# Kernel optimization log

Measured on AMD Instinct MI355X. Metric: run time of the kernel, lower is better.

The kernel has to match this reference:

```python
import jax, jax.numpy as jnp
import numpy as np

IN_FEATURES = 4096
OUT_FEATURES = 16384
BATCH, SEQ = 4, 2048


def setup_inputs() -> dict:
    key = jax.random.key(0)
    k_x, k_w, k_b = jax.random.split(key, 3)
    x = jax.random.normal(k_x, (BATCH, SEQ, IN_FEATURES), dtype=jnp.float32)
    # int8-valued quantized weight stored as int32 for portability (values in [-128, 127])
    weight_quantized = jax.random.randint(k_w, (OUT_FEATURES, IN_FEATURES), -128, 128, dtype=jnp.int32)
    weight_scale = jnp.float32(0.01)        # scalar scale (symmetric quant)
    weight_zero_point = jnp.float32(0.0)    # scalar zero point
    bias = jax.random.normal(k_b, (OUT_FEATURES,), dtype=jnp.float32)
    return {
        "x": x,
        "weight_quantized": weight_quantized,
        "weight_scale": weight_scale,
        "weight_zero_point": weight_zero_point,
        "bias": bias,
    }


def reference(x, weight_quantized, weight_scale, weight_zero_point, bias):
    # dequantize: (q - zero_point) * scale  -> fp32 weight [out, in]
    weight = (weight_quantized.astype(jnp.float32) - weight_zero_point) * weight_scale
    # F.linear: y = x @ W^T + b ; x: [b, s, in], W: [out, in] -> y: [b, s, out]
    return jnp.einsum("bsi,oi->bso", x, weight) + bias
```

## Files before the change

### kernel.cpp

```cpp
#include <hip/hip_runtime.h>
#include <hip/hip_bf16.h>
#include <cstdint>


#define M_DIM 8192
#define N_DIM 16384
#define K_DIM 4096
#define BK    128
#define NT    (K_DIM / BK)

using i32x4 = __attribute__((ext_vector_type(4))) int;

__global__ __launch_bounds__(256) void quant_x_kernel(const float* __restrict__ x,
                                                      signed char* __restrict__ xq,
                                                      float* __restrict__ rs1,
                                                      float* __restrict__ rs2) {
    const int row = blockIdx.x;
    const float* xr = x + (size_t)row * K_DIM;
    const int tid = threadIdx.x;

    float4 v[4];
    float amax = 0.f;
    #pragma unroll
    for (int j = 0; j < 4; ++j) {
        v[j] = *(const float4*)(xr + j * 1024 + tid * 4);
        amax = fmaxf(amax, fmaxf(fmaxf(fabsf(v[j].x), fabsf(v[j].y)),
                                 fmaxf(fabsf(v[j].z), fabsf(v[j].w))));
    }
    #pragma unroll
    for (int off = 32; off > 0; off >>= 1)
        amax = fmaxf(amax, __shfl_xor(amax, off));
    __shared__ float smax[4];
    __shared__ int   ssum[4];
    const int wv = tid >> 6, ln = tid & 63;
    if (ln == 0) smax[wv] = amax;
    __syncthreads();
    amax = fmaxf(fmaxf(smax[0], smax[1]), fmaxf(smax[2], smax[3]));
    const float s   = amax * (1.0f / 127.0f);
    const float inv = amax > 0.f ? 127.0f / amax : 0.f;

    int sum = 0;
    #pragma unroll
    for (int j = 0; j < 4; ++j) {
        int q0 = (int)__builtin_rintf(v[j].x * inv);
        int q1 = (int)__builtin_rintf(v[j].y * inv);
        int q2 = (int)__builtin_rintf(v[j].z * inv);
        int q3 = (int)__builtin_rintf(v[j].w * inv);
        sum += q0 + q1 + q2 + q3;
        int packed = (q0 & 255) | ((q1 & 255) << 8) | ((q2 & 255) << 16) | ((q3 & 255) << 24);
        *(int*)(xq + (size_t)row * K_DIM + j * 1024 + tid * 4) = packed;
    }
    #pragma unroll
    for (int off = 32; off > 0; off >>= 1)
        sum += __shfl_xor(sum, off);
    if (ln == 0) ssum[wv] = sum;
    __syncthreads();
    if (tid == 0) {
        int t = ssum[0] + ssum[1] + ssum[2] + ssum[3];
        rs1[row] = s;
        rs2[row] = s * (float)t;
    }
}

__global__ void quant_w_kernel(const int* __restrict__ q, signed char* __restrict__ o,
                               long long n) {
    long long i = ((long long)blockIdx.x * blockDim.x + threadIdx.x) * 4;
    const long long stride = (long long)gridDim.x * blockDim.x * 4;
    for (; i < n; i += stride) {
        int4 v = *(const int4*)(q + i);
        int packed = (v.x & 255) | ((v.y & 255) << 8) | ((v.z & 255) << 16) | ((v.w & 255) << 24);
        *(int*)(o + i) = packed;
    }
}

#define SB() __builtin_amdgcn_sched_barrier(0)

__device__ __forceinline__ void barrier_() {
    SB();
    asm volatile("" ::: "memory");
    __builtin_amdgcn_s_barrier();
    asm volatile("" ::: "memory");
    SB();
}

__device__ __forceinline__ void stage_half(const signed char* g0, unsigned char* l0) {
    __builtin_amdgcn_global_load_lds((const __attribute__((address_space(1))) void*)g0,
                                     (__attribute__((address_space(3))) void*)l0, 16, 0, 0);
    __builtin_amdgcn_global_load_lds(
        (const __attribute__((address_space(1))) void*)(g0 + (size_t)64 * K_DIM),
        (__attribute__((address_space(3))) void*)(l0 + 8192), 16, 0, 0);
}

__global__ __launch_bounds__(512, 2) void gemm_i8_kernel(const signed char* __restrict__ A,
                                                         const signed char* __restrict__ B,
                                                         const float* __restrict__ rs1,
                                                         const float* __restrict__ rs2,
                                                         const float* __restrict__ scale,
                                                         const float* __restrict__ zpp,
                                                         const float* __restrict__ bias,
                                                         float* __restrict__ C) {
    extern __shared__ unsigned char smem[];

    const int tid  = threadIdx.x;
    const int wave = tid >> 6;
    const int lane = tid & 63;
    const int fr = lane & 15, kq = lane >> 4;
    const int wr = wave >> 2, wc = wave & 3;

    const int swz = (blockIdx.x & 7) * 256 + (blockIdx.x >> 3);
    const int ntn = N_DIM / 256;
    const int tileRow = (swz / ntn) * 256;
    const int tileCol = (swz % ntn) * 256;

    const size_t goff = (size_t)(tid >> 3) * K_DIM + (((tid & 7) ^ ((tid >> 3) & 7)) * 16);
    const signed char* Au  = A + (size_t)tileRow * K_DIM + goff;
    const signed char* Bu  = B + (size_t)tileCol * K_DIM + goff;
    const signed char* AuH = Au + (size_t)128 * K_DIM;
    const signed char* BuH = Bu + (size_t)128 * K_DIM;

    const int aoffB = wr * 16384 + fr * 128;
    const int boffB = 32768 + wc * 8192 + fr * 128;
    int cs[2];
    #pragma unroll
    for (int ks = 0; ks < 2; ++ks)
        cs[ks] = ((ks * 4 + kq) ^ (fr & 7)) * 16;

    i32x4 acc[8][4] = {};
    i32x4 arA[4][2], arB[4][2], b0r[2][2], b1r[2][2];

    {
        unsigned char* w0 = smem + wave * 1024;
        unsigned char* w1 = smem + 65536 + wave * 1024;
        stage_half(Au,  w0);
        stage_half(AuH, w0 + 16384);
        stage_half(Bu,  w0 + 32768);
        stage_half(BuH, w0 + 49152);
        stage_half(Bu + BK,  w1 + 32768);
        stage_half(BuH + BK, w1 + 49152);
        stage_half(Au + BK,  w1);
    }
    SB();
    asm volatile("s_waitcnt vmcnt(6)" ::: "memory");
    barrier_();
    #pragma unroll
    for (int m = 0; m < 4; ++m)
        #pragma unroll
        for (int ks = 0; ks < 2; ++ks)
            arA[m][ks] = *(const i32x4*)(smem + aoffB + m * 2048 + cs[ks]);
    #pragma unroll
    for (int n = 0; n < 2; ++n)
        #pragma unroll
        for (int ks = 0; ks < 2; ++ks)
            b0r[n][ks] = *(const i32x4*)(smem + boffB + n * 2048 + cs[ks]);
    SB();

    for (int t = 0; t < NT; ++t) {
        const unsigned char* sbr = smem + (t & 1) * 65536;
        const unsigned char* nxr = smem + ((t + 1) & 1) * 65536;
        unsigned char* sbw = smem + (t & 1) * 65536 + wave * 1024;
        unsigned char* nxw = smem + ((t + 1) & 1) * 65536 + wave * 1024;
        const int kn1 = (t + 1) * BK, kn2 = (t + 2) * BK;

        if (t + 1 < NT) stage_half(AuH + kn1, nxw + 16384);
        #pragma unroll
        for (int n = 0; n < 2; ++n)
            #pragma unroll
            for (int ks = 0; ks < 2; ++ks)
                b1r[n][ks] = *(const i32x4*)(sbr + boffB + (n + 2) * 2048 + cs[ks]);
        SB();
        asm volatile("s_waitcnt lgkmcnt(4)" ::: "memory");
        SB();
        __builtin_amdgcn_s_setprio(1);
        #pragma unroll
        for (int ks = 0; ks < 2; ++ks)
            #pragma unroll
            for (int m = 0; m < 4; ++m)
                #pragma unroll
                for (int n = 0; n < 2; ++n)
                    acc[m][n] = __builtin_amdgcn_mfma_i32_16x16x64_i8(arA[m][ks], b0r[n][ks], acc[m][n], 0, 0, 0);
        __builtin_amdgcn_s_setprio(0);
        barrier_();

        #pragma unroll
        for (int m = 0; m < 4; ++m)
            #pragma unroll
            for (int ks = 0; ks < 2; ++ks)
                arB[m][ks] = *(const i32x4*)(sbr + aoffB + (m + 4) * 2048 + cs[ks]);
        SB();
        asm volatile("s_waitcnt lgkmcnt(8)" ::: "memory");
        SB();
        __builtin_amdgcn_s_setprio(1);
        #pragma unroll
        for (int ks = 0; ks < 2; ++ks)
            #pragma unroll
            for (int m = 0; m < 4; ++m)
                #pragma unroll
                for (int n = 0; n < 2; ++n)
                    acc[m][n + 2] = __builtin_amdgcn_mfma_i32_16x16x64_i8(arA[m][ks], b1r[n][ks], acc[m][n + 2], 0, 0, 0);
        __builtin_amdgcn_s_setprio(0);
        barrier_();

        if (t + 2 < NT) {
            stage_half(Bu + kn2,  sbw + 32768);
            stage_half(BuH + kn2, sbw + 49152);
        }
        SB();
        asm volatile("s_waitcnt lgkmcnt(0)" ::: "memory");
        SB();
        __builtin_amdgcn_s_setprio(1);
        #pragma unroll
        for (int ks = 0; ks < 2; ++ks)
            #pragma unroll
            for (int m = 0; m < 4; ++m)
                #pragma unroll
                for (int n = 0; n < 2; ++n)
                    acc[m + 4][n + 2] = __builtin_amdgcn_mfma_i32_16x16x64_i8(arB[m][ks], b1r[n][ks], acc[m + 4][n + 2], 0, 0, 0);
        __builtin_amdgcn_s_setprio(0);
        SB();
        if (t + 2 < NT) {
            asm volatile("s_waitcnt vmcnt(4)" ::: "memory");
        } else if (t + 1 < NT) {
            asm volatile("s_waitcnt vmcnt(0)" ::: "memory");
        }
        barrier_();

        if (t + 1 < NT) {
            #pragma unroll
            for (int m = 0; m < 4; ++m)
                #pragma unroll
                for (int ks = 0; ks < 2; ++ks)
                    arA[m][ks] = *(const i32x4*)(nxr + aoffB + m * 2048 + cs[ks]);
        }
        if (t + 2 < NT) stage_half(Au + kn2, sbw);
        SB();
        __builtin_amdgcn_s_setprio(1);
        #pragma unroll
        for (int ks = 0; ks < 2; ++ks)
            #pragma unroll
            for (int m = 0; m < 4; ++m)
                #pragma unroll
                for (int n = 0; n < 2; ++n)
                    acc[m + 4][n] = __builtin_amdgcn_mfma_i32_16x16x64_i8(arB[m][ks], b0r[n][ks], acc[m + 4][n], 0, 0, 0);
        __builtin_amdgcn_s_setprio(0);
        if (t + 1 < NT) {
            #pragma unroll
            for (int n = 0; n < 2; ++n)
                #pragma unroll
                for (int ks = 0; ks < 2; ++ks)
                    b0r[n][ks] = *(const i32x4*)(nxr + boffB + n * 2048 + cs[ks]);
        }
        SB();
        barrier_();
    }

    const float sw  = scale[0];
    const float zpv = zpp[0];
    float bv[4];
    #pragma unroll
    for (int n = 0; n < 4; ++n)
        bv[n] = bias[tileCol + wc * 64 + n * 16 + fr];
    #pragma unroll
    for (int m = 0; m < 8; ++m) {
        #pragma unroll
        for (int j = 0; j < 4; ++j) {
            const int grow = tileRow + wr * 128 + m * 16 + kq * 4 + j;
            const float f1 = rs1[grow] * sw;
            const float f2 = zpv * rs2[grow] * sw;
            float* Crow = C + (size_t)grow * N_DIM + tileCol + wc * 64 + fr;
            #pragma unroll
            for (int n = 0; n < 4; ++n)
                Crow[n * 16] = f1 * (float)acc[m][n][j] - f2 + bv[n];
        }
    }
}

__global__ void gemm_naive(const float* __restrict__ x, const int* __restrict__ wq,
                           const float* __restrict__ sp, const float* __restrict__ zp,
                           const float* __restrict__ bias, float* __restrict__ out) {
    __shared__ float sX[32][33];
    __shared__ float sW[32][33];
    const float s = sp[0], z = zp[0];
    const int tx = threadIdx.x & 15, ty = threadIdx.x >> 4;
    const int row0 = blockIdx.y * 32, col0 = blockIdx.x * 32;
    float acc[2][2] = {};
    for (int k0 = 0; k0 < K_DIM; k0 += 32) {
        for (int i = threadIdx.x; i < 32 * 32; i += 256) {
            int r = i >> 5, cc2 = i & 31;
            sX[r][cc2] = x[(size_t)(row0 + r) * K_DIM + k0 + cc2];
            sW[r][cc2] = ((float)wq[(size_t)(col0 + r) * K_DIM + k0 + cc2] - z) * s;
        }
        __syncthreads();
        #pragma unroll
        for (int k = 0; k < 32; ++k) {
            float xa0 = sX[ty * 2][k], xa1 = sX[ty * 2 + 1][k];
            float wb0 = sW[tx * 2][k], wb1 = sW[tx * 2 + 1][k];
            acc[0][0] += xa0 * wb0; acc[0][1] += xa0 * wb1;
            acc[1][0] += xa1 * wb0; acc[1][1] += xa1 * wb1;
        }
        __syncthreads();
    }
    #pragma unroll
    for (int i = 0; i < 2; ++i)
        #pragma unroll
        for (int j = 0; j < 2; ++j)
            out[(size_t)(row0 + ty * 2 + i) * N_DIM + (col0 + tx * 2 + j)] =
                acc[i][j] + bias[col0 + tx * 2 + j];
}

extern "C" void kernel_launch(void* const* d_in, const int* in_sizes, int n_in,
                              void* d_out, int out_size, void* d_ws, size_t ws_size,
                              hipStream_t stream) {
    const float* x     = (const float*)d_in[0];
    const int*   wq    = (const int*)d_in[1];
    const float* scale = (const float*)d_in[2];
    const float* zp    = (const float*)d_in[3];
    const float* bias  = (const float*)d_in[4];
    float* out = (float*)d_out;

    const size_t offXq = 0;
    const size_t offWq = (size_t)M_DIM * K_DIM;
    const size_t offR1 = offWq + (size_t)N_DIM * K_DIM;
    const size_t offR2 = offR1 + (size_t)M_DIM * sizeof(float);
    const size_t need  = offR2 + (size_t)M_DIM * sizeof(float);

    if (ws_size >= need) {
        signed char* xq  = (signed char*)d_ws + offXq;
        signed char* wq8 = (signed char*)d_ws + offWq;
        float* rs1 = (float*)((char*)d_ws + offR1);
        float* rs2 = (float*)((char*)d_ws + offR2);
        quant_x_kernel<<<M_DIM, 256, 0, stream>>>(x, xq, rs1, rs2);
        quant_w_kernel<<<4096, 256, 0, stream>>>(wq, wq8, (long long)N_DIM * K_DIM);
        (void)hipFuncSetAttribute((const void*)gemm_i8_kernel,
                                  hipFuncAttributeMaxDynamicSharedMemorySize, 131072);
        gemm_i8_kernel<<<(M_DIM / 256) * (N_DIM / 256), 512, 131072, stream>>>(
            xq, wq8, rs1, rs2, scale, zp, bias, out);
    } else {
        dim3 grid(N_DIM / 32, M_DIM / 32);
        gemm_naive<<<grid, 256, 0, stream>>>(x, wq, scale, zp, bias, out);
    }
}
```

Before: 640.3 us.

## Load B fragments directly from global into registers, bypassing LDS, and remap tile grid

The weight (B) operand is no longer staged through shared memory. Each wave loads its own MFMA B fragments straight from global memory into registers one k-tile ahead, which halves LDS use to 64 KB and removes the B LDS reads and writes. The tile mapping is also changed so each XCD owns a contiguous band of output columns, with rows varying fastest, to improve L2 reuse of B. In exchange, B global loads are no longer shared within the block: the four wave-rows read duplicate data, so B traffic into L1/L2 rises and the loads are small strided 16-byte reads. The vmcnt waits are reworked to match the new load counts.

```diff
diff --git a/kernel.cpp b/kernel.cpp
--- a/kernel.cpp
+++ b/kernel.cpp
@@ -107,68 +107,69 @@
     const int fr = lane & 15, kq = lane >> 4;
     const int wr = wave >> 2, wc = wave & 3;
 
-    const int swz = (blockIdx.x & 7) * 256 + (blockIdx.x >> 3);
-    const int ntn = N_DIM / 256;
-    const int tileRow = (swz / ntn) * 256;
-    const int tileCol = (swz % ntn) * 256;
+    const int xcd = blockIdx.x & 7, idx = blockIdx.x >> 3;
+    const int tileRow = (idx & 31) * 256;
+    const int tileCol = (xcd * 8 + (idx >> 5)) * 256;
 
     const size_t goff = (size_t)(tid >> 3) * K_DIM + (((tid & 7) ^ ((tid >> 3) & 7)) * 16);
     const signed char* Au  = A + (size_t)tileRow * K_DIM + goff;
-    const signed char* Bu  = B + (size_t)tileCol * K_DIM + goff;
     const signed char* AuH = Au + (size_t)128 * K_DIM;
-    const signed char* BuH = Bu + (size_t)128 * K_DIM;
 
     const int aoffB = wr * 16384 + fr * 128;
-    const int boffB = 32768 + wc * 8192 + fr * 128;
     int cs[2];
     #pragma unroll
     for (int ks = 0; ks < 2; ++ks)
         cs[ks] = ((ks * 4 + kq) ^ (fr & 7)) * 16;
 
+    const signed char* Bv = B + (size_t)(tileCol + wc * 64 + fr) * K_DIM + kq * 16;
+
     i32x4 acc[8][4] = {};
-    i32x4 arA[4][2], arB[4][2], b0r[2][2], b1r[2][2];
+    i32x4 arA[4][2], arB[4][2], bg0[2][2], bg1[2][2];
 
     {
         unsigned char* w0 = smem + wave * 1024;
-        unsigned char* w1 = smem + 65536 + wave * 1024;
+        unsigned char* w1 = smem + 32768 + wave * 1024;
         stage_half(Au,  w0);
         stage_half(AuH, w0 + 16384);
-        stage_half(Bu,  w0 + 32768);
-        stage_half(BuH, w0 + 49152);
-        stage_half(Bu + BK,  w1 + 32768);
-        stage_half(BuH + BK, w1 + 49152);
-        stage_half(Au + BK,  w1);
+        SB();
+        #pragma unroll
+        for (int n = 0; n < 2; ++n)
+            #pragma unroll
+            for (int ks = 0; ks < 2; ++ks)
+                bg0[n][ks] = *(const i32x4*)(Bv + (size_t)(n) * 16 * K_DIM + ks * 64);
+        #pragma unroll
+        for (int n = 0; n < 2; ++n)
+            #pragma unroll
+            for (int ks = 0; ks < 2; ++ks)
+                bg1[n][ks] = *(const i32x4*)(Bv + (size_t)(n + 2) * 16 * K_DIM + ks * 64);
+        SB();
+        stage_half(Au + BK, w1);
     }
     SB();
-    asm volatile("s_waitcnt vmcnt(6)" ::: "memory");
+    asm volatile("s_waitcnt vmcnt(10)" ::: "memory");
     barrier_();
     #pragma unroll
     for (int m = 0; m < 4; ++m)
         #pragma unroll
         for (int ks = 0; ks < 2; ++ks)
             arA[m][ks] = *(const i32x4*)(smem + aoffB + m * 2048 + cs[ks]);
-    #pragma unroll
-    for (int n = 0; n < 2; ++n)
-        #pragma unroll
-        for (int ks = 0; ks < 2; ++ks)
-            b0r[n][ks] = *(const i32x4*)(smem + boffB + n * 2048 + cs[ks]);
     SB();
 
     for (int t = 0; t < NT; ++t) {
-        const unsigned char* sbr = smem + (t & 1) * 65536;
-        const unsigned char* nxr = smem + ((t + 1) & 1) * 65536;
-        unsigned char* sbw = smem + (t & 1) * 65536 + wave * 1024;
-        unsigned char* nxw = smem + ((t + 1) & 1) * 65536 + wave * 1024;
+        const unsigned char* sbr = smem + (t & 1) * 32768;
+        const unsigned char* nxr = smem + ((t + 1) & 1) * 32768;
+        unsigned char* sbw = smem + (t & 1) * 32768 + wave * 1024;
+        unsigned char* nxw = smem + ((t + 1) & 1) * 32768 + wave * 1024;
         const int kn1 = (t + 1) * BK, kn2 = (t + 2) * BK;
 
         if (t + 1 < NT) stage_half(AuH + kn1, nxw + 16384);
-        #pragma unroll
-        for (int n = 0; n < 2; ++n)
-            #pragma unroll
-            for (int ks = 0; ks < 2; ++ks)
-                b1r[n][ks] = *(const i32x4*)(sbr + boffB + (n + 2) * 2048 + cs[ks]);
-        SB();
-        asm volatile("s_waitcnt lgkmcnt(4)" ::: "memory");
+        SB();
+        asm volatile("s_waitcnt lgkmcnt(0)" ::: "memory");
+        if (t + 1 < NT) {
+            asm volatile("s_waitcnt vmcnt(8)" ::: "memory");
+        } else {
+            asm volatile("s_waitcnt vmcnt(4)" ::: "memory");
+        }
         SB();
         __builtin_amdgcn_s_setprio(1);
         #pragma unroll
@@ -177,7 +178,7 @@
             for (int m = 0; m < 4; ++m)
                 #pragma unroll
                 for (int n = 0; n < 2; ++n)
-                    acc[m][n] = __builtin_amdgcn_mfma_i32_16x16x64_i8(arA[m][ks], b0r[n][ks], acc[m][n], 0, 0, 0);
+                    acc[m][n] = __builtin_amdgcn_mfma_i32_16x16x64_i8(arA[m][ks], bg0[n][ks], acc[m][n], 0, 0, 0);
         __builtin_amdgcn_s_setprio(0);
         barrier_();
 
@@ -187,7 +188,11 @@
             for (int ks = 0; ks < 2; ++ks)
                 arB[m][ks] = *(const i32x4*)(sbr + aoffB + (m + 4) * 2048 + cs[ks]);
         SB();
-        asm volatile("s_waitcnt lgkmcnt(8)" ::: "memory");
+        if (t + 1 < NT) {
+            asm volatile("s_waitcnt vmcnt(4)" ::: "memory");
+        } else {
+            asm volatile("s_waitcnt vmcnt(0)" ::: "memory");
+        }
         SB();
         __builtin_amdgcn_s_setprio(1);
         #pragma unroll
@@ -196,14 +201,10 @@
             for (int m = 0; m < 4; ++m)
                 #pragma unroll
                 for (int n = 0; n < 2; ++n)
-                    acc[m][n + 2] = __builtin_amdgcn_mfma_i32_16x16x64_i8(arA[m][ks], b1r[n][ks], acc[m][n + 2], 0, 0, 0);
+                    acc[m][n + 2] = __builtin_amdgcn_mfma_i32_16x16x64_i8(arA[m][ks], bg1[n][ks], acc[m][n + 2], 0, 0, 0);
         __builtin_amdgcn_s_setprio(0);
         barrier_();
 
-        if (t + 2 < NT) {
-            stage_half(Bu + kn2,  sbw + 32768);
-            stage_half(BuH + kn2, sbw + 49152);
-        }
         SB();
         asm volatile("s_waitcnt lgkmcnt(0)" ::: "memory");
         SB();
@@ -214,14 +215,10 @@
             for (int m = 0; m < 4; ++m)
                 #pragma unroll
                 for (int n = 0; n < 2; ++n)
-                    acc[m + 4][n + 2] = __builtin_amdgcn_mfma_i32_16x16x64_i8(arB[m][ks], b1r[n][ks], acc[m + 4][n + 2], 0, 0, 0);
+                    acc[m + 4][n + 2] = __builtin_amdgcn_mfma_i32_16x16x64_i8(arB[m][ks], bg1[n][ks], acc[m + 4][n + 2], 0, 0, 0);
         __builtin_amdgcn_s_setprio(0);
         SB();
-        if (t + 2 < NT) {
-            asm volatile("s_waitcnt vmcnt(4)" ::: "memory");
-        } else if (t + 1 < NT) {
-            asm volatile("s_waitcnt vmcnt(0)" ::: "memory");
-        }
+        asm volatile("s_waitcnt vmcnt(0)" ::: "memory");
         barrier_();
 
         if (t + 1 < NT) {
@@ -231,24 +228,31 @@
                 for (int ks = 0; ks < 2; ++ks)
                     arA[m][ks] = *(const i32x4*)(nxr + aoffB + m * 2048 + cs[ks]);
         }
+        SB();
+        __builtin_amdgcn_s_setprio(1);
+        #pragma unroll
+        for (int ks = 0; ks < 2; ++ks)
+            #pragma unroll
+            for (int m = 0; m < 4; ++m)
+                #pragma unroll
+                for (int n = 0; n < 2; ++n)
+                    acc[m + 4][n] = __builtin_amdgcn_mfma_i32_16x16x64_i8(arB[m][ks], bg0[n][ks], acc[m + 4][n], 0, 0, 0);
+        __builtin_amdgcn_s_setprio(0);
+        SB();
+        if (t + 1 < NT) {
+            #pragma unroll
+            for (int n = 0; n < 2; ++n)
+                #pragma unroll
+                for (int ks = 0; ks < 2; ++ks)
+                    bg0[n][ks] = *(const i32x4*)(Bv + (size_t)(n) * 16 * K_DIM + ks * 64 + kn1);
+            #pragma unroll
+            for (int n = 0; n < 2; ++n)
+                #pragma unroll
+                for (int ks = 0; ks < 2; ++ks)
+                    bg1[n][ks] = *(const i32x4*)(Bv + (size_t)(n + 2) * 16 * K_DIM + ks * 64 + kn1);
+        }
+        SB();
         if (t + 2 < NT) stage_half(Au + kn2, sbw);
-        SB();
-        __builtin_amdgcn_s_setprio(1);
-        #pragma unroll
-        for (int ks = 0; ks < 2; ++ks)
-            #pragma unroll
-            for (int m = 0; m < 4; ++m)
-                #pragma unroll
-                for (int n = 0; n < 2; ++n)
-                    acc[m + 4][n] = __builtin_amdgcn_mfma_i32_16x16x64_i8(arB[m][ks], b0r[n][ks], acc[m + 4][n], 0, 0, 0);
-        __builtin_amdgcn_s_setprio(0);
-        if (t + 1 < NT) {
-            #pragma unroll
-            for (int n = 0; n < 2; ++n)
-                #pragma unroll
-                for (int ks = 0; ks < 2; ++ks)
-                    b0r[n][ks] = *(const i32x4*)(nxr + boffB + n * 2048 + cs[ks]);
-        }
         SB();
         barrier_();
     }
@@ -331,8 +335,8 @@
         quant_x_kernel<<<M_DIM, 256, 0, stream>>>(x, xq, rs1, rs2);
         quant_w_kernel<<<4096, 256, 0, stream>>>(wq, wq8, (long long)N_DIM * K_DIM);
         (void)hipFuncSetAttribute((const void*)gemm_i8_kernel,
-                                  hipFuncAttributeMaxDynamicSharedMemorySize, 131072);
-        gemm_i8_kernel<<<(M_DIM / 256) * (N_DIM / 256), 512, 131072, stream>>>(
+                                  hipFuncAttributeMaxDynamicSharedMemorySize, 65536);
+        gemm_i8_kernel<<<(M_DIM / 256) * (N_DIM / 256), 512, 65536, stream>>>(
             xq, wq8, rs1, rs2, scale, zp, bias, out);
     } else {
         dim3 grid(N_DIM / 32, M_DIM / 32);
```

Result: slower. 1.130 ms (+76.5%).

## Restructure int8 GEMM to 256x128 tiles, 4 waves, BK=64 double-buffered LDS

Applied to the files above, without the earlier changes.

Replaces the 256x256 tile, 8-wave, BK=128 int8 GEMM with a 256x128 tile, 4-wave, BK=64 kernel. Each wave now computes 128x64, and LDS per block drops from 128KB to 48KB, so more blocks can reside per CU. The pipeline is simplified to two MFMA phases per K-step with fewer barriers. The cost is lower arithmetic intensity per block, since each B tile is reused across only 256 rows and each A tile across only 128 columns, plus twice as many K iterations with their own sync overhead.

```diff
diff --git a/kernel.cpp b/kernel.cpp
--- a/kernel.cpp
+++ b/kernel.cpp
@@ -6,7 +6,7 @@
 #define M_DIM 8192
 #define N_DIM 16384
 #define K_DIM 4096
-#define BK    128
+#define BK    64
 #define NT    (K_DIM / BK)
 
 using i32x4 = __attribute__((ext_vector_type(4))) int;
@@ -83,15 +83,22 @@
     SB();
 }
 
-__device__ __forceinline__ void stage_half(const signed char* g0, unsigned char* l0) {
-    __builtin_amdgcn_global_load_lds((const __attribute__((address_space(1))) void*)g0,
-                                     (__attribute__((address_space(3))) void*)l0, 16, 0, 0);
-    __builtin_amdgcn_global_load_lds(
-        (const __attribute__((address_space(1))) void*)(g0 + (size_t)64 * K_DIM),
-        (__attribute__((address_space(3))) void*)(l0 + 8192), 16, 0, 0);
-}
-
-__global__ __launch_bounds__(512, 2) void gemm_i8_kernel(const signed char* __restrict__ A,
+__device__ __forceinline__ void stage_A4(const signed char* g0, unsigned char* l0) {
+    #pragma unroll
+    for (int j = 0; j < 4; ++j)
+        __builtin_amdgcn_global_load_lds(
+            (const __attribute__((address_space(1))) void*)(g0 + (size_t)(j * 64) * K_DIM),
+            (__attribute__((address_space(3))) void*)(l0 + j * 4096), 16, 0, 0);
+}
+__device__ __forceinline__ void stage_B2(const signed char* g0, unsigned char* l0) {
+    #pragma unroll
+    for (int j = 0; j < 2; ++j)
+        __builtin_amdgcn_global_load_lds(
+            (const __attribute__((address_space(1))) void*)(g0 + (size_t)(j * 64) * K_DIM),
+            (__attribute__((address_space(3))) void*)(l0 + j * 4096), 16, 0, 0);
+}
+
+__global__ __launch_bounds__(256, 2) void gemm_i8_kernel(const signed char* __restrict__ A,
                                                          const signed char* __restrict__ B,
                                                          const float* __restrict__ rs1,
                                                          const float* __restrict__ rs2,
@@ -105,116 +112,73 @@
     const int wave = tid >> 6;
     const int lane = tid & 63;
     const int fr = lane & 15, kq = lane >> 4;
-    const int wr = wave >> 2, wc = wave & 3;
-
-    const int swz = (blockIdx.x & 7) * 256 + (blockIdx.x >> 3);
-    const int ntn = N_DIM / 256;
-    const int tileRow = (swz / ntn) * 256;
-    const int tileCol = (swz % ntn) * 256;
-
-    const size_t goff = (size_t)(tid >> 3) * K_DIM + (((tid & 7) ^ ((tid >> 3) & 7)) * 16);
-    const signed char* Au  = A + (size_t)tileRow * K_DIM + goff;
-    const signed char* Bu  = B + (size_t)tileCol * K_DIM + goff;
-    const signed char* AuH = Au + (size_t)128 * K_DIM;
-    const signed char* BuH = Bu + (size_t)128 * K_DIM;
-
-    const int aoffB = wr * 16384 + fr * 128;
-    const int boffB = 32768 + wc * 8192 + fr * 128;
-    int cs[2];
-    #pragma unroll
-    for (int ks = 0; ks < 2; ++ks)
-        cs[ks] = ((ks * 4 + kq) ^ (fr & 7)) * 16;
+    const int wr = wave >> 1, wc = wave & 1;
+
+    const int swz = (blockIdx.x & 7) * 512 + (blockIdx.x >> 3);
+    const int tileRow = (swz & 31) * 256;
+    const int tileCol = (swz >> 5) * 128;
+
+    const size_t goff = (size_t)(tid >> 2) * K_DIM + (((tid & 3) ^ ((tid >> 3) & 3)) * 16);
+    const signed char* Au = A + (size_t)tileRow * K_DIM + goff;
+    const signed char* Bu = B + (size_t)tileCol * K_DIM + goff;
+
+    const int cs   = (kq ^ ((fr >> 1) & 3)) * 16;
+    const int aoff = wr * 8192 + fr * 64 + cs;
+    const int boff = 16384 + wc * 4096 + fr * 64 + cs;
 
     i32x4 acc[8][4] = {};
-    i32x4 arA[4][2], arB[4][2], b0r[2][2], b1r[2][2];
+    i32x4 arA[8], b0r[2], b1r[2];
 
     {
         unsigned char* w0 = smem + wave * 1024;
-        unsigned char* w1 = smem + 65536 + wave * 1024;
-        stage_half(Au,  w0);
-        stage_half(AuH, w0 + 16384);
-        stage_half(Bu,  w0 + 32768);
-        stage_half(BuH, w0 + 49152);
-        stage_half(Bu + BK,  w1 + 32768);
-        stage_half(BuH + BK, w1 + 49152);
-        stage_half(Au + BK,  w1);
+        unsigned char* w1 = smem + 24576 + wave * 1024;
+        stage_A4(Au,      w0);
+        stage_B2(Bu,      w0 + 16384);
+        stage_A4(Au + BK, w1);
     }
     SB();
-    asm volatile("s_waitcnt vmcnt(6)" ::: "memory");
+    asm volatile("s_waitcnt vmcnt(4)" ::: "memory");
     barrier_();
-    #pragma unroll
-    for (int m = 0; m < 4; ++m)
-        #pragma unroll
-        for (int ks = 0; ks < 2; ++ks)
-            arA[m][ks] = *(const i32x4*)(smem + aoffB + m * 2048 + cs[ks]);
-    #pragma unroll
-    for (int n = 0; n < 2; ++n)
-        #pragma unroll
-        for (int ks = 0; ks < 2; ++ks)
-            b0r[n][ks] = *(const i32x4*)(smem + boffB + n * 2048 + cs[ks]);
-    SB();
 
     for (int t = 0; t < NT; ++t) {
-        const unsigned char* sbr = smem + (t & 1) * 65536;
-        const unsigned char* nxr = smem + ((t + 1) & 1) * 65536;
-        unsigned char* sbw = smem + (t & 1) * 65536 + wave * 1024;
-        unsigned char* nxw = smem + ((t + 1) & 1) * 65536 + wave * 1024;
-        const int kn1 = (t + 1) * BK, kn2 = (t + 2) * BK;
-
-        if (t + 1 < NT) stage_half(AuH + kn1, nxw + 16384);
+        const unsigned char* cb = smem + (t & 1) * 24576;
+        unsigned char* cw = smem + (t & 1) * 24576 + wave * 1024;
+        unsigned char* nw = smem + ((t + 1) & 1) * 24576 + wave * 1024;
+
+        #pragma unroll
+        for (int m = 0; m < 8; ++m)
+            arA[m] = *(const i32x4*)(cb + aoff + m * 1024);
         #pragma unroll
         for (int n = 0; n < 2; ++n)
+            b0r[n] = *(const i32x4*)(cb + boff + n * 1024);
+        SB();
+        #pragma unroll
+        for (int n = 0; n < 2; ++n)
+            b1r[n] = *(const i32x4*)(cb + boff + (n + 2) * 1024);
+        SB();
+        if (t + 1 < NT) stage_B2(Bu + (t + 1) * BK, nw + 16384);
+        SB();
+        asm volatile("s_waitcnt lgkmcnt(2)" ::: "memory");
+        SB();
+        __builtin_amdgcn_s_setprio(1);
+        #pragma unroll
+        for (int m = 0; m < 8; ++m)
             #pragma unroll
-            for (int ks = 0; ks < 2; ++ks)
-                b1r[n][ks] = *(const i32x4*)(sbr + boffB + (n + 2) * 2048 + cs[ks]);
-        SB();
-        asm volatile("s_waitcnt lgkmcnt(4)" ::: "memory");
-        SB();
-        __builtin_amdgcn_s_setprio(1);
-        #pragma unroll
-        for (int ks = 0; ks < 2; ++ks)
-            #pragma unroll
-            for (int m = 0; m < 4; ++m)
-                #pragma unroll
-                for (int n = 0; n < 2; ++n)
-                    acc[m][n] = __builtin_amdgcn_mfma_i32_16x16x64_i8(arA[m][ks], b0r[n][ks], acc[m][n], 0, 0, 0);
+            for (int n = 0; n < 2; ++n)
+                acc[m][n] = __builtin_amdgcn_mfma_i32_16x16x64_i8(arA[m], b0r[n], acc[m][n], 0, 0, 0);
         __builtin_amdgcn_s_setprio(0);
         barrier_();
 
-        #pragma unroll
-        for (int m = 0; m < 4; ++m)
+        if (t + 2 < NT) stage_A4(Au + (t + 2) * BK, cw);
+        SB();
+        asm volatile("s_waitcnt lgkmcnt(0)" ::: "memory");
+        SB();
+        __builtin_amdgcn_s_setprio(1);
+        #pragma unroll
+        for (int m = 0; m < 8; ++m)
             #pragma unroll
-            for (int ks = 0; ks < 2; ++ks)
-                arB[m][ks] = *(const i32x4*)(sbr + aoffB + (m + 4) * 2048 + cs[ks]);
-        SB();
-        asm volatile("s_waitcnt lgkmcnt(8)" ::: "memory");
-        SB();
-        __builtin_amdgcn_s_setprio(1);
-        #pragma unroll
-        for (int ks = 0; ks < 2; ++ks)
-            #pragma unroll
-            for (int m = 0; m < 4; ++m)
-                #pragma unroll
-                for (int n = 0; n < 2; ++n)
-                    acc[m][n + 2] = __builtin_amdgcn_mfma_i32_16x16x64_i8(arA[m][ks], b1r[n][ks], acc[m][n + 2], 0, 0, 0);
-        __builtin_amdgcn_s_setprio(0);
-        barrier_();
-
-        if (t + 2 < NT) {
-            stage_half(Bu + kn2,  sbw + 32768);
-            stage_half(BuH + kn2, sbw + 49152);
-        }
-        SB();
-        asm volatile("s_waitcnt lgkmcnt(0)" ::: "memory");
-        SB();
-        __builtin_amdgcn_s_setprio(1);
-        #pragma unroll
-        for (int ks = 0; ks < 2; ++ks)
-            #pragma unroll
-            for (int m = 0; m < 4; ++m)
-                #pragma unroll
-                for (int n = 0; n < 2; ++n)
-                    acc[m + 4][n + 2] = __builtin_amdgcn_mfma_i32_16x16x64_i8(arB[m][ks], b1r[n][ks], acc[m + 4][n + 2], 0, 0, 0);
+            for (int n = 0; n < 2; ++n)
+                acc[m][n + 2] = __builtin_amdgcn_mfma_i32_16x16x64_i8(arA[m], b1r[n], acc[m][n + 2], 0, 0, 0);
         __builtin_amdgcn_s_setprio(0);
         SB();
         if (t + 2 < NT) {
@@ -222,34 +186,6 @@
         } else if (t + 1 < NT) {
             asm volatile("s_waitcnt vmcnt(0)" ::: "memory");
         }
-        barrier_();
-
-        if (t + 1 < NT) {
-            #pragma unroll
-            for (int m = 0; m < 4; ++m)
-                #pragma unroll
-                for (int ks = 0; ks < 2; ++ks)
-                    arA[m][ks] = *(const i32x4*)(nxr + aoffB + m * 2048 + cs[ks]);
-        }
-        if (t + 2 < NT) stage_half(Au + kn2, sbw);
-        SB();
-        __builtin_amdgcn_s_setprio(1);
-        #pragma unroll
-        for (int ks = 0; ks < 2; ++ks)
-            #pragma unroll
-            for (int m = 0; m < 4; ++m)
-                #pragma unroll
-                for (int n = 0; n < 2; ++n)
-                    acc[m + 4][n] = __builtin_amdgcn_mfma_i32_16x16x64_i8(arB[m][ks], b0r[n][ks], acc[m + 4][n], 0, 0, 0);
-        __builtin_amdgcn_s_setprio(0);
-        if (t + 1 < NT) {
-            #pragma unroll
-            for (int n = 0; n < 2; ++n)
-                #pragma unroll
-                for (int ks = 0; ks < 2; ++ks)
-                    b0r[n][ks] = *(const i32x4*)(nxr + boffB + n * 2048 + cs[ks]);
-        }
-        SB();
         barrier_();
     }
 
@@ -331,8 +267,8 @@
         quant_x_kernel<<<M_DIM, 256, 0, stream>>>(x, xq, rs1, rs2);
         quant_w_kernel<<<4096, 256, 0, stream>>>(wq, wq8, (long long)N_DIM * K_DIM);
         (void)hipFuncSetAttribute((const void*)gemm_i8_kernel,
-                                  hipFuncAttributeMaxDynamicSharedMemorySize, 131072);
-        gemm_i8_kernel<<<(M_DIM / 256) * (N_DIM / 256), 512, 131072, stream>>>(
+                                  hipFuncAttributeMaxDynamicSharedMemorySize, 49152);
+        gemm_i8_kernel<<<(M_DIM / 256) * (N_DIM / 128), 256, 49152, stream>>>(
             xq, wq8, rs1, rs2, scale, zp, bias, out);
     } else {
         dim3 grid(N_DIM / 32, M_DIM / 32);
```

New measurement: 899.7 us. 40.5% more time.
